# Kernel tuning notes

Hardware: AMD Instinct MI355X
Metric: run time of the kernel (lower is better)

The kernel has to match this reference:

```python
import jax, jax.numpy as jnp
import numpy as np

EPS = 1e-5
C1 = 64


def conv2d(x, w, pad):
    return jax.lax.conv_general_dilated(x, w, (1, 1), [(pad, pad), (pad, pad)],
                                        dimension_numbers=('NCHW', 'OIHW', 'NCHW'))


def batchnorm(x, scale, bias, mean, var):
    # inference-mode BN with running stats
    inv = scale * jax.lax.rsqrt(var + EPS)
    return x * inv[None, :, None, None] + (bias - mean * inv)[None, :, None, None]


def _interp_mat(n_out, n_in):
    # 1-D bilinear interpolation matrix, align_corners=True
    pos = jnp.linspace(0.0, n_in - 1.0, n_out)
    i0 = jnp.clip(jnp.floor(pos).astype(jnp.int32), 0, n_in - 1)
    i1 = jnp.clip(i0 + 1, 0, n_in - 1)
    w1 = pos - i0.astype(pos.dtype)
    r = jnp.arange(n_out)
    M = jnp.zeros((n_out, n_in), jnp.float32)
    M = M.at[r, i0].add(1.0 - w1).at[r, i1].add(w1)
    return M


def resize_ac(x, oh, ow):
    # bilinear resize with align_corners=True (matches F.interpolate/UpsamplingBilinear2d)
    Mh = _interp_mat(oh, x.shape[2])
    Mw = _interp_mat(ow, x.shape[3])
    return jnp.einsum('pw,nchw,oh->ncop', Mw, x, Mh)


def grid_sample_bilinear(img, grid):
    # img [N,C,H,W]; grid [N,Ho,Wo,2] (x,y) in [-1,1]; align_corners=False, zeros padding
    N, C, H, W = img.shape
    x = (grid[..., 0] + 1.0) * (W * 0.5) - 0.5
    y = (grid[..., 1] + 1.0) * (H * 0.5) - 0.5
    x0 = jnp.floor(x)
    y0 = jnp.floor(y)
    x1 = x0 + 1.0
    y1 = y0 + 1.0
    wx1 = x - x0
    wy1 = y - y0

    def gather(im, yi, xi):
        # im [C,H,W]; yi,xi [Ho,Wo] float pixel coords
        valid = (xi >= 0) & (xi <= W - 1) & (yi >= 0) & (yi <= H - 1)
        xc = jnp.clip(xi, 0, W - 1).astype(jnp.int32)
        yc = jnp.clip(yi, 0, H - 1).astype(jnp.int32)
        return im[:, yc, xc] * valid[None].astype(im.dtype)

    def sample_one(im, x0, x1, y0, y1, wx1, wy1):
        return (gather(im, y0, x0) * ((1 - wy1) * (1 - wx1))[None]
                + gather(im, y0, x1) * ((1 - wy1) * wx1)[None]
                + gather(im, y1, x0) * (wy1 * (1 - wx1))[None]
                + gather(im, y1, x1) * (wy1 * wx1)[None])

    return jax.vmap(sample_one)(img, x0, x1, y0, y1, wx1, wy1)


def warp(inp, out_h, out_w, delta):
    # build base grid exactly like bilinear_interpolate_torch_gridsample
    N, C, H, W = inp.shape
    ys = jnp.linspace(-1.0, 1.0, out_h)
    xs = jnp.linspace(-1.0, 1.0, out_w)
    gx = jnp.broadcast_to(xs[None, :], (out_h, out_w))
    gy = jnp.broadcast_to(ys[:, None], (out_h, out_w))
    base = jnp.stack([gx, gy], axis=-1)[None]  # [1,Ho,Wo,2]
    norm = jnp.array([W, H], inp.dtype)  # delta[...,0]/W, delta[...,1]/H
    grid = base + jnp.transpose(delta, (0, 2, 3, 1)) / norm
    return grid_sample_bilinear(inp, grid)


def forward(low_stage, high_stage, in_map,
            dg1_w1, dg1_scale, dg1_bias, dg1_mean, dg1_var, dg1_w2,
            dg2_w1, dg2_scale, dg2_bias, dg2_mean, dg2_var, dg2_w2,
            gamma, out_w, out_b):
    h, w = low_stage.shape[2], low_stage.shape[3]
    high = resize_ac(high_stage, h, w)
    imap = jax.nn.sigmoid(resize_ac(in_map, in_map.shape[2] * 2, in_map.shape[3] * 2))
    cat = jnp.concatenate([low_stage, high], axis=1)  # [N,2*C1,h,w]
    d1 = conv2d(batchnorm(conv2d(cat, dg1_w1, 0), dg1_scale, dg1_bias, dg1_mean, dg1_var), dg1_w2, 1)
    d2 = conv2d(batchnorm(conv2d(cat, dg2_w1, 0), dg2_scale, dg2_bias, dg2_mean, dg2_var), dg2_w2, 1)
    hi = warp(high, h, w, d1)
    lo = warp(low_stage, h, w, d2)
    hs = hi + lo
    f = gamma * hs * imap + hs
    o = conv2d(f, out_w, 1) + out_b[None, :, None, None]
    return f, o


def setup_inputs() -> dict:
    key = jax.random.key(0)
    ks = jax.random.split(key, 24)
    N, H, W = 8, 160, 160
    d = {}
    d['low_stage'] = jax.random.normal(ks[0], (N, C1, H, W), jnp.float32)
    d['high_stage'] = jax.random.normal(ks[1], (N, C1, H // 2, W // 2), jnp.float32)
    d['in_map'] = jax.random.normal(ks[2], (N, 1, H // 2, W // 2), jnp.float32)

    def bnp(k):
        k1, k2, k3, k4 = jax.random.split(k, 4)
        return (jax.random.normal(k1, (C1,)) * 0.1 + 1.0,
                jax.random.normal(k2, (C1,)) * 0.1,
                jax.random.normal(k3, (C1,)) * 0.1,
                jax.random.uniform(k4, (C1,), minval=0.5, maxval=1.5))

    for i, p in ((3, 'dg1'), (10, 'dg2')):
        d[p + '_w1'] = jax.random.normal(ks[i], (C1, 2 * C1, 1, 1), jnp.float32) * 0.05
        s, b, m, v = bnp(ks[i + 1])
        d[p + '_scale'], d[p + '_bias'], d[p + '_mean'], d[p + '_var'] = s, b, m, v
        d[p + '_w2'] = jax.random.normal(ks[i + 2], (2, C1, 3, 3), jnp.float32) * 0.05
    d['gamma'] = jnp.ones((1,), jnp.float32)
    d['out_w'] = jax.random.normal(ks[20], (1, C1, 3, 3), jnp.float32) * 0.05
    d['out_b'] = jnp.zeros((1,), jnp.float32)
    return d


def reference(low_stage, high_stage, in_map,
              dg1_w1, dg1_scale, dg1_bias, dg1_mean, dg1_var, dg1_w2,
              dg2_w1, dg2_scale, dg2_bias, dg2_mean, dg2_var, dg2_w2,
              gamma, out_w, out_b):
    return forward(low_stage, high_stage, in_map,
                   dg1_w1, dg1_scale, dg1_bias, dg1_mean, dg1_var, dg1_w2,
                   dg2_w1, dg2_scale, dg2_bias, dg2_mean, dg2_var, dg2_w2,
                   gamma, out_w, out_b)
```

## Files before the change

### kernel.cpp

```cpp
#include <hip/hip_runtime.h>
#include <cmath>

#define N_   8
#define C_   64
#define H_   160
#define W_   160
#define HW_  25600
#define HH_  80
#define WH_  80
#define FSZ_ (N_ * C_ * HW_)
#define PSZ_ (N_ * HW_)

typedef unsigned short ushort8v __attribute__((ext_vector_type(8)));
typedef short          bf16x8  __attribute__((ext_vector_type(8)));
typedef float          f32x4   __attribute__((ext_vector_type(4)));

__device__ __forceinline__ float bf2f(unsigned short u) {
    return __uint_as_float(((unsigned)u) << 16);
}
__device__ __forceinline__ unsigned short f2bf(float f) {
    unsigned u = __float_as_uint(f);
    u += 0x7FFF + ((u >> 16) & 1);
    return (unsigned short)(u >> 16);
}

__device__ __forceinline__ void gs_setup(float bgx, float bgy, float dx, float dy,
                                         int* idx, float* wgt)
{
    float px = ((bgx + dx * (1.f / 160.f)) + 1.f) * 80.f - 0.5f;
    float py = ((bgy + dy * (1.f / 160.f)) + 1.f) * 80.f - 0.5f;
    float x0f = floorf(px), y0f = floorf(py);
    float wx1 = px - x0f, wy1 = py - y0f, wx0 = 1.f - wx1, wy0 = 1.f - wy1;
    int x0 = (int)x0f, y0 = (int)y0f;
    float mx0 = ((unsigned)x0       < (unsigned)W_) ? 1.f : 0.f;
    float mx1 = ((unsigned)(x0 + 1) < (unsigned)W_) ? 1.f : 0.f;
    float my0 = ((unsigned)y0       < (unsigned)H_) ? 1.f : 0.f;
    float my1 = ((unsigned)(y0 + 1) < (unsigned)H_) ? 1.f : 0.f;
    int x0c = min(max(x0, 0), W_ - 1), x1c = min(max(x0 + 1, 0), W_ - 1);
    int y0c = min(max(y0, 0), H_ - 1), y1c = min(max(y0 + 1, 0), H_ - 1);
    idx[0] = y0c * W_ + x0c; wgt[0] = wy0 * wx0 * my0 * mx0;
    idx[1] = y0c * W_ + x1c; wgt[1] = wy0 * wx1 * my0 * mx1;
    idx[2] = y1c * W_ + x0c; wgt[2] = wy1 * wx0 * my1 * mx0;
    idx[3] = y1c * W_ + x1c; wgt[3] = wy1 * wx1 * my1 * mx1;
}

__global__ __launch_bounds__(128) void compose_w_kernel(
    const float* __restrict__ w1a, const float* __restrict__ w1b,
    const float* __restrict__ s1, const float* __restrict__ b1,
    const float* __restrict__ m1, const float* __restrict__ v1,
    const float* __restrict__ s2, const float* __restrict__ b2,
    const float* __restrict__ m2, const float* __restrict__ v2,
    const float* __restrict__ w2a, const float* __restrict__ w2b,
    float* __restrict__ weffg, float* __restrict__ btap4)
{
    __shared__ float ws2[64], bpart[64];
    int bId = blockIdx.x;
    int row = bId / 9, tap = bId % 9;
    int br = row >> 1, oc = row & 1;
    int tid = threadIdx.x;

    const float* w1 = br ? w1b : w1a;
    const float* w2 = br ? w2b : w2a;

    if (tid < 64) {
        int mid = tid;
        float sc = br ? s2[mid] : s1[mid];
        float vv = br ? v2[mid] : v1[mid];
        float bb = br ? b2[mid] : b1[mid];
        float mm = br ? m2[mid] : m1[mid];
        float inv = sc * rsqrtf(vv + 1e-5f);
        float w2v = w2[oc * 576 + mid * 9 + tap];
        ws2[mid]   = w2v * inv;
        bpart[mid] = w2v * (bb - mm * inv);
    }
    __syncthreads();

    float sum = 0.f;
    #pragma unroll 8
    for (int mid = 0; mid < 64; ++mid)
        sum = fmaf(ws2[mid], w1[mid * 128 + tid], sum);
    weffg[(row * 9 + tap) * 128 + tid] = sum;

    if (tid < 64) {
        float part = bpart[tid];
        #pragma unroll
        for (int off = 32; off > 0; off >>= 1)
            part += __shfl_down(part, off);
        if (tid == 0) btap4[tap * 4 + row] = part;
    }
}

__global__ __launch_bounds__(256) void pack_w_kernel(
    const float* __restrict__ weffg, const float* __restrict__ ow,
    unsigned short* __restrict__ wAe, unsigned short* __restrict__ wOe)
{
    int i = blockIdx.x * 256 + threadIdx.x;
    {
        int j    = i & 7;
        int lane = (i >> 3) & 63;
        int s    = (i >> 9) & 3;
        int tap  = i >> 11;
        int row  = lane & 15;
        int ci   = s * 32 + ((lane >> 4) & 3) * 8 + j;
        float v = (row < 4) ? weffg[(row * 9 + tap) * 128 + ci] : 0.f;
        wAe[i] = f2bf(v);
    }
    if (i < 9216) {
        int j    = i & 7;
        int lane = (i >> 3) & 63;
        int s    = (i >> 9) & 1;
        int tap  = i >> 10;
        int row  = lane & 15;
        int ci   = s * 32 + ((lane >> 4) & 3) * 8 + j;
        float v = (row == 0) ? ow[ci * 9 + tap] : 0.f;
        wOe[i] = f2bf(v);
    }
}

__global__ __launch_bounds__(256) void nchw_to_nhwc_bf16(
    const float* __restrict__ in, unsigned short* __restrict__ out, int hw)
{
    int p = blockIdx.x * 256 + threadIdx.x;
    int n = p / hw, rem = p % hw;
    const float* base = in + (long)n * 64 * hw + rem;
    unsigned o32[32];
    #pragma unroll
    for (int c2 = 0; c2 < 32; ++c2) {
        float v0 = base[(long)(2 * c2) * hw];
        float v1 = base[(long)(2 * c2 + 1) * hw];
        o32[c2] = (unsigned)f2bf(v0) | ((unsigned)f2bf(v1) << 16);
    }
    uint4* dst = reinterpret_cast<uint4*>(out + (long)p * 64);
    #pragma unroll
    for (int q = 0; q < 8; ++q)
        dst[q] = make_uint4(o32[q * 4], o32[q * 4 + 1], o32[q * 4 + 2], o32[q * 4 + 3]);
}

__global__ __launch_bounds__(256) void resize_high_nhwc(
    const unsigned short* __restrict__ hsb, unsigned short* __restrict__ highb)
{
    int p = blockIdx.x * 256 + threadIdx.x;
    int n = p / HW_, rem = p % HW_;
    int y = rem / W_, x = rem % W_;
    float sx = (x * 79.0f) / 159.0f;
    float sy = (y * 79.0f) / 159.0f;
    int ix0 = (int)sx, iy0 = (int)sy;
    float fx = sx - (float)ix0, fy = sy - (float)iy0;
    int ix1 = min(ix0 + 1, WH_ - 1), iy1 = min(iy0 + 1, HH_ - 1);
    long b = (long)n * (HH_ * WH_);
    const ushort8v* r00 = (const ushort8v*)(hsb + (b + iy0 * WH_ + ix0) * 64);
    const ushort8v* r01 = (const ushort8v*)(hsb + (b + iy0 * WH_ + ix1) * 64);
    const ushort8v* r10 = (const ushort8v*)(hsb + (b + iy1 * WH_ + ix0) * 64);
    const ushort8v* r11 = (const ushort8v*)(hsb + (b + iy1 * WH_ + ix1) * 64);
    float w00 = (1.f - fx) * (1.f - fy), w01 = fx * (1.f - fy);
    float w10 = (1.f - fx) * fy,         w11 = fx * fy;

    float acc[64];
    #pragma unroll
    for (int c = 0; c < 64; ++c) acc[c] = 0.f;
    #pragma unroll
    for (int q = 0; q < 8; ++q) {
        ushort8v v0 = r00[q], v1 = r01[q], v2 = r10[q], v3 = r11[q];
        #pragma unroll
        for (int j = 0; j < 8; ++j) {
            acc[q * 8 + j] = bf2f(v0[j]) * w00 + bf2f(v1[j]) * w01
                           + bf2f(v2[j]) * w10 + bf2f(v3[j]) * w11;
        }
    }
    unsigned o32[32];
    #pragma unroll
    for (int c2 = 0; c2 < 32; ++c2)
        o32[c2] = (unsigned)f2bf(acc[2 * c2]) | ((unsigned)f2bf(acc[2 * c2 + 1]) << 16);
    uint4* dst = reinterpret_cast<uint4*>(highb + (long)p * 64);
    #pragma unroll
    for (int q = 0; q < 8; ++q)
        dst[q] = make_uint4(o32[q * 4], o32[q * 4 + 1], o32[q * 4 + 2], o32[q * 4 + 3]);
}

__global__ __launch_bounds__(256) void d12_tiled_kernel(
    const unsigned short* __restrict__ lowb, const unsigned short* __restrict__ highb,
    const unsigned short* __restrict__ wAe, const float* __restrict__ btap4,
    float* __restrict__ d1, float* __restrict__ d2)
{
    __shared__ unsigned char lds[46080];
    int b  = blockIdx.x;
    int n  = b / 200;
    int t  = b % 200;
    int ty = t / 10, tx = t % 10;
    int y0 = ty * 8, x0 = tx * 16;
    int tid  = threadIdx.x;
    int lane = tid & 63;
    int wv   = tid >> 6;
    int r16  = lane & 15;
    int quad = lane >> 4;
    long nb = (long)n * HW_;

    for (int i = tid; i < 2880; i += 256) {
        int pix = i >> 4, qq = i & 15;
        int py = pix / 18, px = pix - py * 18;
        int gy = y0 + py - 1, gx = x0 + px - 1;
        bool valid = ((unsigned)gy < (unsigned)H_) && ((unsigned)gx < (unsigned)W_);
        ushort8v v = (ushort8v)0;
        if (valid) {
            const unsigned short* src = (qq < 8) ? lowb : highb;
            v = *reinterpret_cast<const ushort8v*>(
                src + ((long)(nb + gy * W_ + gx)) * 64 + (qq & 7) * 8);
        }
        *reinterpret_cast<ushort8v*>(
            lds + ((pix * 256 + qq * 16) ^ ((pix & 7) << 4))) = v;
    }
    __syncthreads();

    f32x4 accE[2], accO[2];
    accE[0] = accE[1] = accO[0] = accO[1] = (f32x4){0.f, 0.f, 0.f, 0.f};

    #pragma unroll
    for (int kx = 0; kx < 3; ++kx) {
        #pragma unroll
        for (int s = 0; s < 4; ++s) {
            bf16x8 Br[4];
            #pragma unroll
            for (int r = 0; r < 4; ++r) {
                int pix = (wv * 2 + r) * 18 + r16 + kx;
                Br[r] = *reinterpret_cast<const bf16x8*>(
                    lds + ((pix * 256 + s * 64 + quad * 16) ^ ((pix & 7) << 4)));
            }
            #pragma unroll
            for (int ky = 0; ky < 3; ++ky) {
                int tap = ky * 3 + kx;
                bf16x8 A = *reinterpret_cast<const bf16x8*>(
                    wAe + (tap * 4 + s) * 512 + lane * 8);
                if ((tap ^ s) & 1) {
                    accO[0] = __builtin_amdgcn_mfma_f32_16x16x32_bf16(A, Br[ky],     accO[0], 0, 0, 0);
                    accO[1] = __builtin_amdgcn_mfma_f32_16x16x32_bf16(A, Br[ky + 1], accO[1], 0, 0, 0);
                } else {
                    accE[0] = __builtin_amdgcn_mfma_f32_16x16x32_bf16(A, Br[ky],     accE[0], 0, 0, 0);
                    accE[1] = __builtin_amdgcn_mfma_f32_16x16x32_bf16(A, Br[ky + 1], accE[1], 0, 0, 0);
                }
            }
        }
    }

    #pragma unroll
    for (int g = 0; g < 2; ++g) {
        int yg = y0 + wv * 2 + g;
        int x  = x0 + r16;
        bool interior = (yg > 0) && (yg < H_ - 1) && (x0 > 0) && (x0 + 16 < W_);
        float b0 = 0.f, b1v = 0.f, b2v = 0.f, b3 = 0.f;
        #pragma unroll
        for (int tap = 0; tap < 9; ++tap) {
            int ky = tap / 3 - 1, kx = tap % 3 - 1;
            float m = 1.f;
            if (!interior) {
                int yy = yg + ky, xx = x + kx;
                m = (((unsigned)yy < (unsigned)H_) && ((unsigned)xx < (unsigned)W_))
                  ? 1.f : 0.f;
            }
            const float4 bt = *reinterpret_cast<const float4*>(btap4 + tap * 4);
            b0  = fmaf(m, bt.x, b0);
            b1v = fmaf(m, bt.y, b1v);
            b2v = fmaf(m, bt.z, b2v);
            b3  = fmaf(m, bt.w, b3);
        }
        if (quad == 0) {
            long p = nb + (long)yg * W_ + x;
            *reinterpret_cast<float2*>(d1 + p * 2) =
                make_float2(accE[g][0] + accO[g][0] + b0,
                            accE[g][1] + accO[g][1] + b1v);
            *reinterpret_cast<float2*>(d2 + p * 2) =
                make_float2(accE[g][2] + accO[g][2] + b2v,
                            accE[g][3] + accO[g][3] + b3);
        }
    }
}

__global__ __launch_bounds__(256) void warp_out_fused(
    const unsigned short* __restrict__ lowb, const unsigned short* __restrict__ highb,
    const float* __restrict__ d1, const float* __restrict__ d2,
    const float* __restrict__ imin, const float* __restrict__ gamma,
    const unsigned short* __restrict__ wOe, const float* __restrict__ ob,
    float* __restrict__ f, float* __restrict__ o)
{
    __shared__ unsigned char lds[23040];
    int b  = blockIdx.x;
    int n  = b / 200;
    int t  = b % 200;
    int ty = t / 10, tx = t % 10;
    int y0 = ty * 8, x0 = tx * 16;
    int tid  = threadIdx.x;
    long nb = (long)n * HW_;
    float gm = gamma[0];

    for (int u = tid; u < 720; u += 256) {
        int pix = u >> 2, quarter = u & 3;
        int py = pix / 18, px = pix - py * 18;
        int gy = y0 + py - 1, gx = x0 + px - 1;
        bool valid = ((unsigned)gy < (unsigned)H_) && ((unsigned)gx < (unsigned)W_);

        unsigned o32[8];
        #pragma unroll
        for (int k = 0; k < 8; ++k) o32[k] = 0;

        if (valid) {
            int pp = gy * W_ + gx;
            long p = nb + pp;

            float bgx = -1.f + gx * (2.f / 159.f);
            float bgy = -1.f + gy * (2.f / 159.f);
            float2 dv1 = *reinterpret_cast<const float2*>(d1 + p * 2);
            float2 dv2 = *reinterpret_cast<const float2*>(d2 + p * 2);

            int idx1[4], idx2[4];
            float wgt1[4], wgt2[4];
            gs_setup(bgx, bgy, dv1.x, dv1.y, idx1, wgt1);
            gs_setup(bgx, bgy, dv2.x, dv2.y, idx2, wgt2);

            float s;
            {
                float sx = (gx * 79.0f) / 159.0f;
                float sy = (gy * 79.0f) / 159.0f;
                int ix0 = (int)sx, iy0 = (int)sy;
                float fx = sx - (float)ix0, fy = sy - (float)iy0;
                int ix1 = min(ix0 + 1, WH_ - 1), iy1 = min(iy0 + 1, HH_ - 1);
                const float* ip = imin + n * (HH_ * WH_);
                float v00 = ip[iy0 * WH_ + ix0], v01 = ip[iy0 * WH_ + ix1];
                float v10 = ip[iy1 * WH_ + ix0], v11 = ip[iy1 * WH_ + ix1];
                float v = (v00 * (1.f - fx) + v01 * fx) * (1.f - fy)
                        + (v10 * (1.f - fx) + v11 * fx) * fy;
                s = 1.f + gm * (1.f / (1.f + expf(-v)));
            }

            float acc[16];
            #pragma unroll
            for (int c = 0; c < 16; ++c) acc[c] = 0.f;

            #pragma unroll
            for (int j = 0; j < 4; ++j) {
                const ushort8v* row = (const ushort8v*)(
                    highb + (nb + idx1[j]) * 64 + quarter * 16);
                float w = wgt1[j];
                #pragma unroll
                for (int q = 0; q < 2; ++q) {
                    ushort8v v = row[q];
                    #pragma unroll
                    for (int k = 0; k < 8; ++k)
                        acc[q * 8 + k] = fmaf(bf2f(v[k]), w, acc[q * 8 + k]);
                }
            }
            #pragma unroll
            for (int j = 0; j < 4; ++j) {
                const ushort8v* row = (const ushort8v*)(
                    lowb + (nb + idx2[j]) * 64 + quarter * 16);
                float w = wgt2[j];
                #pragma unroll
                for (int q = 0; q < 2; ++q) {
                    ushort8v v = row[q];
                    #pragma unroll
                    for (int k = 0; k < 8; ++k)
                        acc[q * 8 + k] = fmaf(bf2f(v[k]), w, acc[q * 8 + k]);
                }
            }

            bool interior = (py >= 1) && (py <= 8) && (px >= 1) && (px <= 16);
            float* fp = f + (nb + (long)(quarter * 16) * HW_) * 0;
            fp = f + ((long)n * 64 + quarter * 16) * HW_ + pp;
            #pragma unroll
            for (int c2 = 0; c2 < 8; ++c2) {
                float f0 = acc[2 * c2]     * s;
                float f1 = acc[2 * c2 + 1] * s;
                if (interior) {
                    fp[(long)(2 * c2) * HW_]     = f0;
                    fp[(long)(2 * c2 + 1) * HW_] = f1;
                }
                o32[c2] = (unsigned)f2bf(f0) | ((unsigned)f2bf(f1) << 16);
            }
        }

        int base = pix * 128 + quarter * 32;
        int sw   = (pix & 7) << 4;
        *reinterpret_cast<uint4*>(lds + ((base) ^ sw)) =
            make_uint4(o32[0], o32[1], o32[2], o32[3]);
        *reinterpret_cast<uint4*>(lds + ((base + 16) ^ sw)) =
            make_uint4(o32[4], o32[5], o32[6], o32[7]);
    }
    __syncthreads();

    int lane = tid & 63;
    int wv   = tid >> 6;
    int r16  = lane & 15;
    int quad = lane >> 4;

    f32x4 accE[2], accO[2];
    accE[0] = accE[1] = accO[0] = accO[1] = (f32x4){0.f, 0.f, 0.f, 0.f};

    #pragma unroll
    for (int kx = 0; kx < 3; ++kx) {
        #pragma unroll
        for (int s = 0; s < 2; ++s) {
            bf16x8 Br[4];
            #pragma unroll
            for (int r = 0; r < 4; ++r) {
                int pix = (wv * 2 + r) * 18 + r16 + kx;
                Br[r] = *reinterpret_cast<const bf16x8*>(
                    lds + ((pix * 128 + s * 64 + quad * 16) ^ ((pix & 7) << 4)));
            }
            #pragma unroll
            for (int ky = 0; ky < 3; ++ky) {
                int tap = ky * 3 + kx;
                bf16x8 A = *reinterpret_cast<const bf16x8*>(
                    wOe + (tap * 2 + s) * 512 + lane * 8);
                if ((tap ^ s) & 1) {
                    accO[0] = __builtin_amdgcn_mfma_f32_16x16x32_bf16(A, Br[ky],     accO[0], 0, 0, 0);
                    accO[1] = __builtin_amdgcn_mfma_f32_16x16x32_bf16(A, Br[ky + 1], accO[1], 0, 0, 0);
                } else {
                    accE[0] = __builtin_amdgcn_mfma_f32_16x16x32_bf16(A, Br[ky],     accE[0], 0, 0, 0);
                    accE[1] = __builtin_amdgcn_mfma_f32_16x16x32_bf16(A, Br[ky + 1], accE[1], 0, 0, 0);
                }
            }
        }
    }

    if (quad == 0) {
        float bias = ob[0];
        #pragma unroll
        for (int g = 0; g < 2; ++g) {
            int yg = y0 + wv * 2 + g;
            o[nb + (long)yg * W_ + x0 + r16] = accE[g][0] + accO[g][0] + bias;
        }
    }
}

extern "C" void kernel_launch(void* const* d_in, const int* in_sizes, int n_in,
                              void* d_out, int out_size, void* d_ws, size_t ws_size,
                              hipStream_t stream) {
    const float* low    = (const float*)d_in[0];
    const float* hsin   = (const float*)d_in[1];
    const float* imin   = (const float*)d_in[2];
    const float* dg1_w1 = (const float*)d_in[3];
    const float* dg1_s  = (const float*)d_in[4];
    const float* dg1_b  = (const float*)d_in[5];
    const float* dg1_m  = (const float*)d_in[6];
    const float* dg1_v  = (const float*)d_in[7];
    const float* dg1_w2 = (const float*)d_in[8];
    const float* dg2_w1 = (const float*)d_in[9];
    const float* dg2_s  = (const float*)d_in[10];
    const float* dg2_b  = (const float*)d_in[11];
    const float* dg2_m  = (const float*)d_in[12];
    const float* dg2_v  = (const float*)d_in[13];
    const float* dg2_w2 = (const float*)d_in[14];
    const float* gamma  = (const float*)d_in[15];
    const float* out_w  = (const float*)d_in[16];
    const float* out_b  = (const float*)d_in[17];

    float* ws    = (float*)d_ws;
    float* d1    = ws;
    float* d2    = d1 + 2 * PSZ_;
    float* btap4 = d2 + 2 * PSZ_;
    float* weffg = btap4 + 40;
    unsigned short* wAe   = (unsigned short*)(weffg + 4608);
    unsigned short* wOe   = wAe + 18432;
    unsigned short* lowb  = wOe + 9216;
    unsigned short* highb = lowb + FSZ_;
    unsigned short* hsb   = highb + FSZ_;

    float* fout = (float*)d_out;
    float* oout = fout + FSZ_;

    compose_w_kernel<<<36, 128, 0, stream>>>(
        dg1_w1, dg2_w1, dg1_s, dg1_b, dg1_m, dg1_v,
        dg2_s, dg2_b, dg2_m, dg2_v, dg1_w2, dg2_w2, weffg, btap4);
    pack_w_kernel<<<72, 256, 0, stream>>>(weffg, out_w, wAe, wOe);
    nchw_to_nhwc_bf16<<<PSZ_ / 256, 256, 0, stream>>>(low, lowb, HW_);
    nchw_to_nhwc_bf16<<<(N_ * HH_ * WH_) / 256, 256, 0, stream>>>(hsin, hsb, HH_ * WH_);
    resize_high_nhwc<<<PSZ_ / 256, 256, 0, stream>>>(hsb, highb);
    d12_tiled_kernel<<<1600, 256, 0, stream>>>(
        lowb, highb, wAe, btap4, d1, d2);
    warp_out_fused<<<1600, 256, 0, stream>>>(
        lowb, highb, d1, d2, imin, gamma, wOe, out_b, fout, oout);
}
```

Before: 124.2 us.

## Fuse weight packing into compose, merge transposes, enlarge warp-out tiles

The compose kernel now writes the bf16 MFMA-packed weight layouts for both the offset and the output convolutions directly, which removes the separate pack kernel and the fp32 intermediate buffer. The two NCHW-to-NHWC bf16 conversions run in a single launch, with the block index choosing the tensor. The warp/output kernel moves from 8x16 to 16x16 tiles with 512 threads and a larger LDS buffer, so less of the one-pixel halo is recomputed per output pixel and fewer launches are needed. The cost is more LDS per block and a smaller grid of larger blocks, which may lower occupancy.

Result: faster. 119.8 us, median of 2 (-3.6%).

```diff
diff --git a/kernel.cpp b/kernel.cpp
--- a/kernel.cpp
+++ b/kernel.cpp
@@ -51,7 +51,9 @@
     const float* __restrict__ s2, const float* __restrict__ b2,
     const float* __restrict__ m2, const float* __restrict__ v2,
     const float* __restrict__ w2a, const float* __restrict__ w2b,
-    float* __restrict__ weffg, float* __restrict__ btap4)
+    const float* __restrict__ ow,
+    unsigned short* __restrict__ wAe, unsigned short* __restrict__ wOe,
+    float* __restrict__ btap4)
 {
     __shared__ float ws2[64], bpart[64];
     int bId = blockIdx.x;
@@ -79,8 +81,27 @@
     #pragma unroll 8
     for (int mid = 0; mid < 64; ++mid)
         sum = fmaf(ws2[mid], w1[mid * 128 + tid], sum);
-    weffg[(row * 9 + tap) * 128 + tid] = sum;
-
+    {
+        int s = tid >> 5, g = (tid >> 3) & 3, j = tid & 7;
+        wAe[(tap * 4 + s) * 512 + (row + 16 * g) * 8 + j] = f2bf(sum);
+    }
+    if (row == 0) {
+        for (int i = tid; i < 1536; i += 128) {
+            int j = i & 7, k = i >> 3;
+            int s = k / 48, k48 = k % 48;
+            int g = k48 / 12, r16v = 4 + (k48 % 12);
+            wAe[(tap * 4 + s) * 512 + (r16v + 16 * g) * 8 + j] = 0;
+        }
+    }
+    if (row == 1) {
+        for (int i = tid; i < 1024; i += 128) {
+            int j = i & 7, lane = (i >> 3) & 63, s = i >> 9;
+            int rowl = lane & 15;
+            int ci = s * 32 + ((lane >> 4) & 3) * 8 + j;
+            float v = (rowl == 0) ? ow[ci * 9 + tap] : 0.f;
+            wOe[(tap * 2 + s) * 512 + lane * 8 + j] = f2bf(v);
+        }
+    }
     if (tid < 64) {
         float part = bpart[tid];
         #pragma unroll
@@ -90,37 +111,16 @@
     }
 }
 
-__global__ __launch_bounds__(256) void pack_w_kernel(
-    const float* __restrict__ weffg, const float* __restrict__ ow,
-    unsigned short* __restrict__ wAe, unsigned short* __restrict__ wOe)
-{
-    int i = blockIdx.x * 256 + threadIdx.x;
-    {
-        int j    = i & 7;
-        int lane = (i >> 3) & 63;
-        int s    = (i >> 9) & 3;
-        int tap  = i >> 11;
-        int row  = lane & 15;
-        int ci   = s * 32 + ((lane >> 4) & 3) * 8 + j;
-        float v = (row < 4) ? weffg[(row * 9 + tap) * 128 + ci] : 0.f;
-        wAe[i] = f2bf(v);
-    }
-    if (i < 9216) {
-        int j    = i & 7;
-        int lane = (i >> 3) & 63;
-        int s    = (i >> 9) & 1;
-        int tap  = i >> 10;
-        int row  = lane & 15;
-        int ci   = s * 32 + ((lane >> 4) & 3) * 8 + j;
-        float v = (row == 0) ? ow[ci * 9 + tap] : 0.f;
-        wOe[i] = f2bf(v);
-    }
-}
-
-__global__ __launch_bounds__(256) void nchw_to_nhwc_bf16(
-    const float* __restrict__ in, unsigned short* __restrict__ out, int hw)
-{
-    int p = blockIdx.x * 256 + threadIdx.x;
+__global__ __launch_bounds__(256) void nchw_to_nhwc_merged(
+    const float* __restrict__ low, const float* __restrict__ hs,
+    unsigned short* __restrict__ lowb, unsigned short* __restrict__ hsb)
+{
+    int b = blockIdx.x;
+    const float* in;
+    unsigned short* out;
+    int hw, p;
+    if (b < 800) { in = low; out = lowb; hw = HW_;       p = b * 256 + threadIdx.x; }
+    else         { in = hs;  out = hsb;  hw = HH_ * WH_; p = (b - 800) * 256 + threadIdx.x; }
     int n = p / hw, rem = p % hw;
     const float* base = in + (long)n * 64 * hw + rem;
     unsigned o32[32];
@@ -274,24 +274,24 @@
     }
 }
 
-__global__ __launch_bounds__(256) void warp_out_fused(
+__global__ __launch_bounds__(512) void warp_out_fused(
     const unsigned short* __restrict__ lowb, const unsigned short* __restrict__ highb,
     const float* __restrict__ d1, const float* __restrict__ d2,
     const float* __restrict__ imin, const float* __restrict__ gamma,
     const unsigned short* __restrict__ wOe, const float* __restrict__ ob,
     float* __restrict__ f, float* __restrict__ o)
 {
-    __shared__ unsigned char lds[23040];
+    __shared__ unsigned char lds[41472];
     int b  = blockIdx.x;
-    int n  = b / 200;
-    int t  = b % 200;
+    int n  = b / 100;
+    int t  = b % 100;
     int ty = t / 10, tx = t % 10;
-    int y0 = ty * 8, x0 = tx * 16;
+    int y0 = ty * 16, x0 = tx * 16;
     int tid  = threadIdx.x;
     long nb = (long)n * HW_;
     float gm = gamma[0];
 
-    for (int u = tid; u < 720; u += 256) {
+    for (int u = tid; u < 1296; u += 512) {
         int pix = u >> 2, quarter = u & 3;
         int py = pix / 18, px = pix - py * 18;
         int gy = y0 + py - 1, gx = x0 + px - 1;
@@ -361,9 +361,8 @@
                 }
             }
 
-            bool interior = (py >= 1) && (py <= 8) && (px >= 1) && (px <= 16);
-            float* fp = f + (nb + (long)(quarter * 16) * HW_) * 0;
-            fp = f + ((long)n * 64 + quarter * 16) * HW_ + pp;
+            bool interior = (py >= 1) && (py <= 16) && (px >= 1) && (px <= 16);
+            float* fp = f + ((long)n * 64 + quarter * 16) * HW_ + pp;
             #pragma unroll
             for (int c2 = 0; c2 < 8; ++c2) {
                 float f0 = acc[2 * c2]     * s;
@@ -456,8 +455,7 @@
     float* d1    = ws;
     float* d2    = d1 + 2 * PSZ_;
     float* btap4 = d2 + 2 * PSZ_;
-    float* weffg = btap4 + 40;
-    unsigned short* wAe   = (unsigned short*)(weffg + 4608);
+    unsigned short* wAe   = (unsigned short*)(btap4 + 40);
     unsigned short* wOe   = wAe + 18432;
     unsigned short* lowb  = wOe + 9216;
     unsigned short* highb = lowb + FSZ_;
@@ -468,13 +466,12 @@
 
     compose_w_kernel<<<36, 128, 0, stream>>>(
         dg1_w1, dg2_w1, dg1_s, dg1_b, dg1_m, dg1_v,
-        dg2_s, dg2_b, dg2_m, dg2_v, dg1_w2, dg2_w2, weffg, btap4);
-    pack_w_kernel<<<72, 256, 0, stream>>>(weffg, out_w, wAe, wOe);
-    nchw_to_nhwc_bf16<<<PSZ_ / 256, 256, 0, stream>>>(low, lowb, HW_);
-    nchw_to_nhwc_bf16<<<(N_ * HH_ * WH_) / 256, 256, 0, stream>>>(hsin, hsb, HH_ * WH_);
+        dg2_s, dg2_b, dg2_m, dg2_v, dg1_w2, dg2_w2, out_w,
+        wAe, wOe, btap4);
+    nchw_to_nhwc_merged<<<1000, 256, 0, stream>>>(low, hsin, lowb, hsb);
     resize_high_nhwc<<<PSZ_ / 256, 256, 0, stream>>>(hsb, highb);
     d12_tiled_kernel<<<1600, 256, 0, stream>>>(
         lowb, highb, wAe, btap4, d1, d2);
-    warp_out_fused<<<1600, 256, 0, stream>>>(
+    warp_out_fused<<<800, 512, 0, stream>>>(
         lowb, highb, d1, d2, imin, gamma, wOe, out_b, fout, oout);
 }
```
